# Kernel optimization log

Measured on AMD Instinct MI355X. Metric: run time of the kernel, lower is better.

The kernel has to match this reference:

```python
import jax, jax.numpy as jnp
import numpy as np

N, E = 50000, 800000
IN_DIM, H_DIM, OUT_DIM, EDGE_DIM, HEADS = 128, 128, 112, 8, 1
NEG_SLOPE = 0.2
BN_EPS = 1e-5


def _gat_layer(x, src, dst, edge_att, W, a_src, a_dst, We, a_edge, bias):
    """PyG GATConv (concat=False, edge_dim used for attention only)."""
    H, C = a_src.shape  # heads, out channels
    xs = (x @ W).reshape(-1, H, C)            # [N,H,C]
    ef = (edge_att @ We).reshape(-1, H, C)    # [E,H,C]
    al_src = jnp.einsum('nhc,hc->nh', xs, a_src)   # [N,H]
    al_dst = jnp.einsum('nhc,hc->nh', xs, a_dst)   # [N,H]
    al_edge = jnp.einsum('ehc,hc->eh', ef, a_edge) # [E,H]
    alpha = al_src[src] + al_dst[dst] + al_edge    # [E,H]
    alpha = jnp.where(alpha > 0, alpha, NEG_SLOPE * alpha)  # leaky_relu(0.2)
    # segment softmax over incoming edges of each dst node
    m = jax.lax.stop_gradient(jax.ops.segment_max(alpha, dst, num_segments=N))
    ex = jnp.exp(alpha - m[dst])
    den = jax.ops.segment_sum(ex, dst, num_segments=N)
    att = ex / den[dst]                       # [E,H]
    msg = xs[src] * att[:, :, None]           # [E,H,C] gather + weight
    out = jax.ops.segment_sum(msg, dst, num_segments=N)  # scatter-add [N,H,C]
    return out.mean(axis=1) + bias            # concat=False -> head mean


def _batchnorm(h, gamma, beta):
    mu = h.mean(axis=0)
    var = h.var(axis=0)
    return gamma * (h - mu) * jax.lax.rsqrt(var + BN_EPS) + beta


def setup_inputs() -> dict:
    key = jax.random.key(0)
    ks = jax.random.split(key, 20)
    s = 0.1
    inp = {
        'x': jax.random.normal(ks[0], (N, IN_DIM), dtype=jnp.float32),
        'edge_index': jax.random.randint(ks[1], (2, E), 0, N, dtype=jnp.int32),
        'edge_att': jax.random.normal(ks[2], (E, EDGE_DIM), dtype=jnp.float32),
        # layer 0: IN_DIM -> H_DIM
        'W0': s * jax.random.normal(ks[3], (IN_DIM, HEADS * H_DIM), dtype=jnp.float32),
        'a_src0': s * jax.random.normal(ks[4], (HEADS, H_DIM), dtype=jnp.float32),
        'a_dst0': s * jax.random.normal(ks[5], (HEADS, H_DIM), dtype=jnp.float32),
        'We0': s * jax.random.normal(ks[6], (EDGE_DIM, HEADS * H_DIM), dtype=jnp.float32),
        'a_edge0': s * jax.random.normal(ks[7], (HEADS, H_DIM), dtype=jnp.float32),
        'b0': jnp.zeros((H_DIM,), dtype=jnp.float32),
        # layer 1: H_DIM -> OUT_DIM
        'W1': s * jax.random.normal(ks[8], (H_DIM, HEADS * OUT_DIM), dtype=jnp.float32),
        'a_src1': s * jax.random.normal(ks[9], (HEADS, OUT_DIM), dtype=jnp.float32),
        'a_dst1': s * jax.random.normal(ks[10], (HEADS, OUT_DIM), dtype=jnp.float32),
        'We1': s * jax.random.normal(ks[11], (EDGE_DIM, HEADS * OUT_DIM), dtype=jnp.float32),
        'a_edge1': s * jax.random.normal(ks[12], (HEADS, OUT_DIM), dtype=jnp.float32),
        'b1': jnp.zeros((OUT_DIM,), dtype=jnp.float32),
        # batchnorms
        'bn_g': jnp.ones((H_DIM,), dtype=jnp.float32),
        'bn_b': jnp.zeros((H_DIM,), dtype=jnp.float32),
        'bnf_g': jnp.ones((OUT_DIM,), dtype=jnp.float32),
        'bnf_b': jnp.zeros((OUT_DIM,), dtype=jnp.float32),
    }
    return inp


def reference(x, edge_index, edge_att,
              W0, a_src0, a_dst0, We0, a_edge0, b0,
              W1, a_src1, a_dst1, We1, a_edge1, b1,
              bn_g, bn_b, bnf_g, bnf_b):
    src, dst = edge_index[0], edge_index[1]
    h = _gat_layer(x, src, dst, edge_att, W0, a_src0, a_dst0, We0, a_edge0, b0)
    h = _batchnorm(h, bn_g, bn_b)
    h = jax.nn.relu(h)
    # dropout is a no-op in eval; omitted for a deterministic reference
    h = _gat_layer(h, src, dst, edge_att, W1, a_src1, a_dst1, We1, a_edge1, b1)
    h = _batchnorm(h, bnf_g, bnf_b)
    return h
```

## Files before the change

kernel.cpp:

```cpp
#include <hip/hip_runtime.h>
#include <math.h>

#define NN 50000
#define NPAD 50048
#define NE 800000
#define SCAN_B 256
#define SCAN_NBLK ((NN + SCAN_B - 1) / SCAN_B)
#define AGG_NBLK 3200

typedef __attribute__((ext_vector_type(8))) short bf16x8;
typedef __attribute__((ext_vector_type(4))) float f32x4;
typedef __attribute__((ext_vector_type(8))) unsigned short u16x8;

__device__ __forceinline__ unsigned short f2bf(float x) {
    unsigned u = __float_as_uint(x);
    u += 0x7fffu + ((u >> 16) & 1);
    return (unsigned short)(u >> 16);
}
__device__ __forceinline__ float bf2f(unsigned short h) {
    return __uint_as_float(((unsigned)h) << 16);
}

__global__ void k_init_cvt(int* __restrict__ deg, float* __restrict__ stats,
                           const float* __restrict__ We0, const float* __restrict__ ae0,
                           const float* __restrict__ We1, const float* __restrict__ ae1,
                           float* __restrict__ ve,
                           const float* __restrict__ W0, const float* __restrict__ W1,
                           unsigned short* __restrict__ Wth0, unsigned short* __restrict__ Wtl0,
                           unsigned short* __restrict__ Wth1, unsigned short* __restrict__ Wtl1)
{
    int idx = blockIdx.x * 256 + threadIdx.x;
    if (idx < NN) deg[idx] = 0;
    if (idx < 512) stats[idx] = 0.f;
    if (idx < 128 * 128) {
        int k = idx / 128, c = idx % 128;
        float v = W0[idx];
        unsigned short hi = f2bf(v);
        Wth0[c * 128 + k] = hi;
        Wtl0[c * 128 + k] = f2bf(v - bf2f(hi));
    } else if (idx < 128 * 128 + 128 * 112) {
        int i2 = idx - 128 * 128;
        int k = i2 / 112, c = i2 % 112;
        float v = W1[i2];
        unsigned short hi = f2bf(v);
        Wth1[c * 128 + k] = hi;
        Wtl1[c * 128 + k] = f2bf(v - bf2f(hi));
    }
    if (blockIdx.x == gridDim.x - 1) {
        int j = threadIdx.x;
        if (j < 8) {
            float s = 0.f;
            for (int c = 0; c < 128; ++c) s += We0[j * 128 + c] * ae0[c];
            ve[j] = s;
        } else if (j < 16) {
            int jj = j - 8;
            float s = 0.f;
            for (int c = 0; c < 112; ++c) s += We1[jj * 112 + c] * ae1[c];
            ve[8 + jj] = s;
        }
    }
}

__global__ void k_deg(const int* __restrict__ dst, int* __restrict__ deg,
                      int* __restrict__ rank, int E_)
{
    int e = blockIdx.x * blockDim.x + threadIdx.x;
    if (e < E_) rank[e] = atomicAdd(&deg[dst[e]], 1);
}

__global__ void k_scan1(const int* __restrict__ deg, int* __restrict__ partial)
{
    __shared__ int sm[SCAN_B];
    int t = threadIdx.x;
    int idx = blockIdx.x * SCAN_B + t;
    sm[t] = (idx < NN) ? deg[idx] : 0;
    __syncthreads();
    #pragma unroll
    for (int off = SCAN_B / 2; off > 0; off >>= 1) {
        if (t < off) sm[t] += sm[t + off];
        __syncthreads();
    }
    if (t == 0) partial[blockIdx.x] = sm[0];
}

__global__ void k_scan3(const int* __restrict__ deg, const int* __restrict__ partial,
                        int* __restrict__ rp)
{
    __shared__ int sm[SCAN_B];
    __shared__ int pbase;
    int t = threadIdx.x;
    int pv = (t < SCAN_NBLK && t < blockIdx.x) ? partial[t] : 0;
    sm[t] = pv;
    __syncthreads();
    #pragma unroll
    for (int off = SCAN_B / 2; off > 0; off >>= 1) {
        if (t < off) sm[t] += sm[t + off];
        __syncthreads();
    }
    if (t == 0) pbase = sm[0];
    __syncthreads();
    int idx = blockIdx.x * SCAN_B + t;
    int v = (idx < NN) ? deg[idx] : 0;
    sm[t] = v;
    __syncthreads();
    #pragma unroll
    for (int off = 1; off < SCAN_B; off <<= 1) {
        int u = (t >= off) ? sm[t - off] : 0;
        __syncthreads();
        sm[t] += u;
        __syncthreads();
    }
    int excl = pbase + ((t == 0) ? 0 : sm[t - 1]);
    if (idx < NN) rp[idx] = excl;
    if (idx == NN - 1) rp[NN] = excl + v;
}

__global__ void k_csr_fill_l0(const int* __restrict__ src, const int* __restrict__ dst,
                              const float* __restrict__ eatt, const float* __restrict__ ve,
                              const int* __restrict__ rp, const int* __restrict__ rank,
                              const float* __restrict__ als, const float* __restrict__ ald,
                              uint2* __restrict__ pk, int E_)
{
    int i = blockIdx.x * blockDim.x + threadIdx.x;
    int e = i * 2;
    if (e >= E_) return;
    int2 ss = *reinterpret_cast<const int2*>(src + e);
    int2 dd = *reinterpret_cast<const int2*>(dst + e);
    int2 rr = *reinterpret_cast<const int2*>(rank + e);
    const float4* ea = reinterpret_cast<const float4*>(eatt + (size_t)e * 8);
    float4 ea0 = ea[0], ea1 = ea[1], ea2 = ea[2], ea3 = ea[3];

    float a0x = ea0.x * ve[0] + ea0.y * ve[1] + ea0.z * ve[2] + ea0.w * ve[3]
              + ea1.x * ve[4] + ea1.y * ve[5] + ea1.z * ve[6] + ea1.w * ve[7];
    float a1x = ea0.x * ve[8] + ea0.y * ve[9] + ea0.z * ve[10] + ea0.w * ve[11]
              + ea1.x * ve[12] + ea1.y * ve[13] + ea1.z * ve[14] + ea1.w * ve[15];
    float a0y = ea2.x * ve[0] + ea2.y * ve[1] + ea2.z * ve[2] + ea2.w * ve[3]
              + ea3.x * ve[4] + ea3.y * ve[5] + ea3.z * ve[6] + ea3.w * ve[7];
    float a1y = ea2.x * ve[8] + ea2.y * ve[9] + ea2.z * ve[10] + ea2.w * ve[11]
              + ea3.x * ve[12] + ea3.y * ve[13] + ea3.z * ve[14] + ea3.w * ve[15];

    int p0 = rp[dd.x] + rr.x;
    int p1 = rp[dd.y] + rr.y;
    float lx = als[ss.x] + ald[dd.x] + a0x;
    float ly = als[ss.y] + ald[dd.y] + a0y;
    lx = lx > 0.f ? lx : 0.2f * lx;
    ly = ly > 0.f ? ly : 0.2f * ly;

    uint2 r0, r1;
    r0.x = (unsigned)ss.x | ((unsigned)f2bf(a1x) << 16);
    r0.y = __float_as_uint(__expf(lx));
    r1.x = (unsigned)ss.y | ((unsigned)f2bf(a1y) << 16);
    r1.y = __float_as_uint(__expf(ly));
    pk[p0] = r0;
    pk[p1] = r1;
}

template<int COLS, bool BN_IN>
__launch_bounds__(256, 2)
__global__ void k_gemm_mfma(const float* __restrict__ A,
                            const unsigned short* __restrict__ Wth,
                            const unsigned short* __restrict__ Wtl,
                            unsigned short* __restrict__ out,
                            const float* __restrict__ a_src, const float* __restrict__ a_dst,
                            float* __restrict__ als, float* __restrict__ ald,
                            const float* __restrict__ bsum, const float* __restrict__ bsq,
                            const float* __restrict__ gamma, const float* __restrict__ beta)
{
    constexpr int NT = COLS / 16;
    __shared__ unsigned short sBh[COLS * 128];
    __shared__ unsigned short sBl[COLS * 128];
    __shared__ float scN[128], shN[128];

    int wv = threadIdx.x >> 6;
    int lane = threadIdx.x & 63;
    int r0 = blockIdx.x * 64 + wv * 16;
    int m = lane & 15;
    int quad = lane >> 4;
    int arow = r0 + m;
    int rc = (arow < NN) ? arow : NN - 1;
    const float* pa = A + (size_t)rc * 128 + quad * 8;

    float4 av[8];
    #pragma unroll
    for (int ks = 0; ks < 4; ++ks) {
        av[2 * ks]     = *reinterpret_cast<const float4*>(pa + ks * 32);
        av[2 * ks + 1] = *reinterpret_cast<const float4*>(pa + ks * 32 + 4);
    }

    constexpr int CH = COLS * 128 * 2 / 16;
    for (int i = threadIdx.x; i < CH; i += 256) {
        unsigned o = (unsigned)i * 16u;
        unsigned d = o ^ (((o >> 8) & 7u) << 4);
        *reinterpret_cast<uint4*>(reinterpret_cast<char*>(sBh) + d) =
            *reinterpret_cast<const uint4*>(reinterpret_cast<const char*>(Wth) + o);
        *reinterpret_cast<uint4*>(reinterpret_cast<char*>(sBl) + d) =
            *reinterpret_cast<const uint4*>(reinterpret_cast<const char*>(Wtl) + o);
    }
    if (BN_IN) {
        if (threadIdx.x < 128) {
            int k = threadIdx.x;
            float invn = 1.0f / (float)NN;
            float mean = bsum[k] * invn;
            float var  = bsq[k] * invn - mean * mean;
            float sc = gamma[k] * rsqrtf(var + 1e-5f);
            scN[k] = sc;
            shN[k] = beta[k] - mean * sc;
        }
    }
    __syncthreads();

    f32x4 acc[NT];
    #pragma unroll
    for (int t = 0; t < NT; ++t) acc[t] = f32x4{0.f, 0.f, 0.f, 0.f};

    unsigned swz = ((unsigned)(m & 7)) << 4;

    #pragma unroll
    for (int ks = 0; ks < 4; ++ks) {
        float4 v0 = av[2 * ks], v1 = av[2 * ks + 1];
        float vv[8] = {v0.x, v0.y, v0.z, v0.w, v1.x, v1.y, v1.z, v1.w};
        int kb = ks * 32 + quad * 8;
        bf16x8 ah, al;
        #pragma unroll
        for (int jj = 0; jj < 8; ++jj) {
            float f = vv[jj];
            if (BN_IN) f = fmaxf(f * scN[kb + jj] + shN[kb + jj], 0.f);
            unsigned short hi = f2bf(f);
            ah[jj] = (short)hi;
            al[jj] = (short)f2bf(f - bf2f(hi));
        }
        #pragma unroll
        for (int t = 0; t < NT; ++t) {
            int c = t * 16 + m;
            unsigned b = ((unsigned)c * 256u + (unsigned)ks * 64u + (unsigned)quad * 16u) ^ swz;
            bf16x8 bh = *reinterpret_cast<const bf16x8*>(reinterpret_cast<const char*>(sBh) + b);
            bf16x8 bl = *reinterpret_cast<const bf16x8*>(reinterpret_cast<const char*>(sBl) + b);
            acc[t] = __builtin_amdgcn_mfma_f32_16x16x32_bf16(ah, bh, acc[t], 0, 0, 0);
            acc[t] = __builtin_amdgcn_mfma_f32_16x16x32_bf16(al, bh, acc[t], 0, 0, 0);
            acc[t] = __builtin_amdgcn_mfma_f32_16x16x32_bf16(ah, bl, acc[t], 0, 0, 0);
        }
    }

    float p[4] = {0.f, 0.f, 0.f, 0.f}, q[4] = {0.f, 0.f, 0.f, 0.f};
    #pragma unroll
    for (int t = 0; t < NT; ++t) {
        int c = t * 16 + m;
        float asv = a_src[c], adv = a_dst[c];
        #pragma unroll
        for (int rI = 0; rI < 4; ++rI) {
            float v = acc[t][rI];
            int row = r0 + quad * 4 + rI;
            if (row < NN) out[(size_t)row * COLS + c] = f2bf(v);
            p[rI] += v * asv;
            q[rI] += v * adv;
        }
    }
    #pragma unroll
    for (int rI = 0; rI < 4; ++rI) {
        #pragma unroll
        for (int off = 1; off <= 8; off <<= 1) {
            p[rI] += __shfl_xor(p[rI], off);
            q[rI] += __shfl_xor(q[rI], off);
        }
    }
    if (m == 0) {
        #pragma unroll
        for (int rI = 0; rI < 4; ++rI) {
            int row = r0 + quad * 4 + rI;
            if (row < NN) { als[row] = p[rI]; ald[row] = q[rI]; }
        }
    }
}

__global__ void k_logit1(const int* __restrict__ rp, const uint2* __restrict__ pk,
                         const float* __restrict__ als, const float* __restrict__ ald,
                         uint2* __restrict__ pe1)
{
    int ql = threadIdx.x & 15;
    int w = blockIdx.x * 16 + (threadIdx.x >> 4);
    if (w >= NN) return;
    int beg = rp[w], end = rp[w + 1];
    float aldv = ald[w];
    for (int p = beg + ql; p < end; p += 16) {
        uint2 r = pk[p];
        float a = als[r.x & 0xffffu] + aldv + bf2f((unsigned short)(r.x >> 16));
        a = a > 0.f ? a : 0.2f * a;
        uint2 o;
        o.x = r.x;
        o.y = __float_as_uint(__expf(a));
        pe1[p] = o;
    }
}

template<int COLS>
__global__ void k_aggregate(const int* __restrict__ rp, const uint2* __restrict__ pe,
                            const unsigned short* __restrict__ xs, float* __restrict__ out,
                            float* __restrict__ psum, float* __restrict__ psq)
{
    __shared__ float sS[16 * 128], sQ[16 * 128];
    int ql = threadIdx.x & 15;
    int wq = threadIdx.x >> 4;
    int col = ql * 8;
    bool act = (col < COLS);
    int qid = blockIdx.x * 16 + wq;
    float bs[8] = {0.f,0.f,0.f,0.f,0.f,0.f,0.f,0.f};
    float bq[8] = {0.f,0.f,0.f,0.f,0.f,0.f,0.f,0.f};

    for (int w = qid; w < NN; w += AGG_NBLK * 16) {
        int beg = rp[w], end = rp[w + 1];
        float acc[8] = {0.f,0.f,0.f,0.f,0.f,0.f,0.f,0.f};
        float den = 0.f;
        int j = beg;
        for (; j + 8 <= end; j += 8) {
            uint2 r0 = pe[j],     r1 = pe[j + 1], r2 = pe[j + 2], r3 = pe[j + 3];
            uint2 r4 = pe[j + 4], r5 = pe[j + 5], r6 = pe[j + 6], r7 = pe[j + 7];
            float e0 = __uint_as_float(r0.y), e1 = __uint_as_float(r1.y);
            float e2 = __uint_as_float(r2.y), e3 = __uint_as_float(r3.y);
            float e4 = __uint_as_float(r4.y), e5 = __uint_as_float(r5.y);
            float e6 = __uint_as_float(r6.y), e7 = __uint_as_float(r7.y);
            den += ((e0 + e1) + (e2 + e3)) + ((e4 + e5) + (e6 + e7));
            if (act) {
                u16x8 u0 = *reinterpret_cast<const u16x8*>(xs + (size_t)(r0.x & 0xffffu) * COLS + col);
                u16x8 u1 = *reinterpret_cast<const u16x8*>(xs + (size_t)(r1.x & 0xffffu) * COLS + col);
                u16x8 u2 = *reinterpret_cast<const u16x8*>(xs + (size_t)(r2.x & 0xffffu) * COLS + col);
                u16x8 u3 = *reinterpret_cast<const u16x8*>(xs + (size_t)(r3.x & 0xffffu) * COLS + col);
                u16x8 u4 = *reinterpret_cast<const u16x8*>(xs + (size_t)(r4.x & 0xffffu) * COLS + col);
                u16x8 u5 = *reinterpret_cast<const u16x8*>(xs + (size_t)(r5.x & 0xffffu) * COLS + col);
                u16x8 u6 = *reinterpret_cast<const u16x8*>(xs + (size_t)(r6.x & 0xffffu) * COLS + col);
                u16x8 u7 = *reinterpret_cast<const u16x8*>(xs + (size_t)(r7.x & 0xffffu) * COLS + col);
                #pragma unroll
                for (int k = 0; k < 8; ++k)
                    acc[k] += (((e0 * bf2f(u0[k]) + e1 * bf2f(u1[k]))
                              + (e2 * bf2f(u2[k]) + e3 * bf2f(u3[k])))
                             + ((e4 * bf2f(u4[k]) + e5 * bf2f(u5[k]))
                              + (e6 * bf2f(u6[k]) + e7 * bf2f(u7[k]))));
            }
        }
        if (j < end) {
            bool v1 = j + 1 < end, v2 = j + 2 < end, v3 = j + 3 < end;
            bool v4 = j + 4 < end, v5 = j + 5 < end, v6 = j + 6 < end;
            uint2 r0 = pe[j];
            uint2 r1 = v1 ? pe[j + 1] : uint2{0u, 0u};
            uint2 r2 = v2 ? pe[j + 2] : uint2{0u, 0u};
            uint2 r3 = v3 ? pe[j + 3] : uint2{0u, 0u};
            uint2 r4 = v4 ? pe[j + 4] : uint2{0u, 0u};
            uint2 r5 = v5 ? pe[j + 5] : uint2{0u, 0u};
            uint2 r6 = v6 ? pe[j + 6] : uint2{0u, 0u};
            float e0 = __uint_as_float(r0.y), e1 = __uint_as_float(r1.y);
            float e2 = __uint_as_float(r2.y), e3 = __uint_as_float(r3.y);
            float e4 = __uint_as_float(r4.y), e5 = __uint_as_float(r5.y);
            float e6 = __uint_as_float(r6.y);
            den += ((e0 + e1) + (e2 + e3)) + ((e4 + e5) + e6);
            if (act) {
                u16x8 u0 = *reinterpret_cast<const u16x8*>(xs + (size_t)(r0.x & 0xffffu) * COLS + col);
                #pragma unroll
                for (int k = 0; k < 8; ++k) acc[k] += e0 * bf2f(u0[k]);
                if (v1) {
                    u16x8 u = *reinterpret_cast<const u16x8*>(xs + (size_t)(r1.x & 0xffffu) * COLS + col);
                    #pragma unroll
                    for (int k = 0; k < 8; ++k) acc[k] += e1 * bf2f(u[k]);
                }
                if (v2) {
                    u16x8 u = *reinterpret_cast<const u16x8*>(xs + (size_t)(r2.x & 0xffffu) * COLS + col);
                    #pragma unroll
                    for (int k = 0; k < 8; ++k) acc[k] += e2 * bf2f(u[k]);
                }
                if (v3) {
                    u16x8 u = *reinterpret_cast<const u16x8*>(xs + (size_t)(r3.x & 0xffffu) * COLS + col);
                    #pragma unroll
                    for (int k = 0; k < 8; ++k) acc[k] += e3 * bf2f(u[k]);
                }
                if (v4) {
                    u16x8 u = *reinterpret_cast<const u16x8*>(xs + (size_t)(r4.x & 0xffffu) * COLS + col);
                    #pragma unroll
                    for (int k = 0; k < 8; ++k) acc[k] += e4 * bf2f(u[k]);
                }
                if (v5) {
                    u16x8 u = *reinterpret_cast<const u16x8*>(xs + (size_t)(r5.x & 0xffffu) * COLS + col);
                    #pragma unroll
                    for (int k = 0; k < 8; ++k) acc[k] += e5 * bf2f(u[k]);
                }
                if (v6) {
                    u16x8 u = *reinterpret_cast<const u16x8*>(xs + (size_t)(r6.x & 0xffffu) * COLS + col);
                    #pragma unroll
                    for (int k = 0; k < 8; ++k) acc[k] += e6 * bf2f(u[k]);
                }
            }
        }
        float inv = (end > beg) ? 1.f / den : 0.f;
        if (act) {
            float o[8];
            #pragma unroll
            for (int k = 0; k < 8; ++k) {
                o[k] = acc[k] * inv;
                bs[k] += o[k];
                bq[k] += o[k] * o[k];
            }
            f32x4 o0 = {o[0], o[1], o[2], o[3]};
            f32x4 o1 = {o[4], o[5], o[6], o[7]};
            __builtin_nontemporal_store(o0, reinterpret_cast<f32x4*>(out + (size_t)w * COLS + col));
            __builtin_nontemporal_store(o1, reinterpret_cast<f32x4*>(out + (size_t)w * COLS + col + 4));
        }
    }
    #pragma unroll
    for (int k = 0; k < 8; ++k) {
        sS[wq * 128 + col + k] = act ? bs[k] : 0.f;
        sQ[wq * 128 + col + k] = act ? bq[k] : 0.f;
    }
    __syncthreads();
    int t = threadIdx.x;
    if (t < 128) {
        float s = 0.f, s2 = 0.f;
        #pragma unroll
        for (int r = 0; r < 16; ++r) { s += sS[r * 128 + t]; s2 += sQ[r * 128 + t]; }
        psum[(size_t)blockIdx.x * 128 + t] = s;
        psq [(size_t)blockIdx.x * 128 + t] = s2;
    }
}

__global__ void k_bn_stats2(const float* __restrict__ psum, const float* __restrict__ psq,
                            float* __restrict__ sums, float* __restrict__ sqs)
{
    int t = threadIdx.x;
    int c = t & 127;
    constexpr int ROWS = AGG_NBLK / 128;
    const float* sp = (t < 128) ? psum : psq;
    float s = 0.f;
    #pragma unroll 5
    for (int i = 0; i < ROWS; ++i)
        s += sp[(size_t)(blockIdx.x * ROWS + i) * 128 + c];
    unsafeAtomicAdd(((t < 128) ? sums : sqs) + c, s);
}

template<int COLS>
__global__ void k_bn_apply(const float* __restrict__ in, float* __restrict__ out,
                           const float* __restrict__ sums, const float* __restrict__ sqs,
                           const float* __restrict__ gamma, const float* __restrict__ beta,
                           int n)
{
    int idx = blockIdx.x * blockDim.x + threadIdx.x;
    if (idx >= n * COLS) return;
    int c = idx % COLS;
    float invn = 1.0f / (float)n;
    float mean = sums[c] * invn;
    float var  = sqs[c] * invn - mean * mean;
    float sc = gamma[c] * rsqrtf(var + 1e-5f);
    float sh = beta[c] - mean * sc;
    out[idx] = in[idx] * sc + sh;
}

extern "C" void kernel_launch(void* const* d_in, const int* in_sizes, int n_in,
                              void* d_out, int out_size, void* d_ws, size_t ws_size,
                              hipStream_t stream)
{
    const float* x    = (const float*)d_in[0];
    const int*   eidx = (const int*)d_in[1];
    const float* eatt = (const float*)d_in[2];
    const float* W0   = (const float*)d_in[3];
    const float* as0  = (const float*)d_in[4];
    const float* ad0  = (const float*)d_in[5];
    const float* We0  = (const float*)d_in[6];
    const float* ae0  = (const float*)d_in[7];
    const float* W1   = (const float*)d_in[9];
    const float* as1  = (const float*)d_in[10];
    const float* ad1  = (const float*)d_in[11];
    const float* We1  = (const float*)d_in[12];
    const float* ae1  = (const float*)d_in[13];
    const float* bng  = (const float*)d_in[15];
    const float* bnb  = (const float*)d_in[16];
    const float* bnfg = (const float*)d_in[17];
    const float* bnfb = (const float*)d_in[18];

    const int N = NN, E = NE;
    const int* src = eidx;
    const int* dst = eidx + E;

    float* ws = (float*)d_ws;
    size_t off = 0;
    unsigned short* xs0b = (unsigned short*)(ws + off); off += (size_t)N * 64;
    float* h   = ws + off;      off += (size_t)N * 128;
    unsigned short* xs1b = (unsigned short*)(ws + off); off += (size_t)N * 56;
    uint2* pk = (uint2*)(ws + off);     off += (size_t)E * 2;
    int*   rp   = (int*)(ws + off);     off += N + 2;
    float* als0 = ws + off;     off += N;
    float* ald0 = ws + off;     off += N;
    float* als1 = ws + off;     off += N;
    float* ald1 = ws + off;     off += N;
    float* stats = ws + off;    off += 512;
    float* ve = ws + off;       off += 16;
    int*   partial = (int*)(ws + off);  off += SCAN_NBLK;
    float* psum = ws + off;     off += (size_t)AGG_NBLK * 128;
    float* psq  = ws + off;     off += (size_t)AGG_NBLK * 128;
    unsigned short* Wth0 = (unsigned short*)(ws + off); off += 128 * 64;
    unsigned short* Wtl0 = (unsigned short*)(ws + off); off += 128 * 64;
    unsigned short* Wth1 = (unsigned short*)(ws + off); off += 112 * 64;
    unsigned short* Wtl1 = (unsigned short*)(ws + off); off += 112 * 64;

    int*   rank = (int*)h;
    int*   deg  = (int*)(h + 800000);
    uint2* pe1  = (uint2*)xs0b;
    float* out1 = h;

    float* sum0 = stats;
    float* sq0  = stats + 128;
    float* sum1 = stats + 256;
    float* sq1  = stats + 384;

    k_init_cvt<<<(N + 255) / 256, 256, 0, stream>>>(deg, stats, We0, ae0, We1, ae1, ve,
                                                    W0, W1, Wth0, Wtl0, Wth1, Wtl1);

    k_deg<<<(E + 255) / 256, 256, 0, stream>>>(dst, deg, rank, E);
    k_scan1<<<SCAN_NBLK, SCAN_B, 0, stream>>>(deg, partial);
    k_scan3<<<SCAN_NBLK, SCAN_B, 0, stream>>>(deg, partial, rp);

    k_gemm_mfma<128, false><<<NPAD / 64, 256, 0, stream>>>(x, Wth0, Wtl0, xs0b,
                                                           as0, ad0, als0, ald0,
                                                           nullptr, nullptr, nullptr, nullptr);
    k_csr_fill_l0<<<(E / 2 + 255) / 256, 256, 0, stream>>>(src, dst, eatt, ve, rp, rank,
                                                           als0, ald0, pk, E);
    k_aggregate<128><<<AGG_NBLK, 256, 0, stream>>>(rp, pk, xs0b, h, psum, psq);
    k_bn_stats2<<<128, 256, 0, stream>>>(psum, psq, sum0, sq0);

    k_gemm_mfma<112, true><<<NPAD / 64, 256, 0, stream>>>(h, Wth1, Wtl1, xs1b,
                                                          as1, ad1, als1, ald1,
                                                          sum0, sq0, bng, bnb);
    k_logit1<<<(N + 15) / 16, 256, 0, stream>>>(rp, pk, als1, ald1, pe1);
    k_aggregate<112><<<AGG_NBLK, 256, 0, stream>>>(rp, pe1, xs1b, out1, psum, psq);
    k_bn_stats2<<<128, 256, 0, stream>>>(psum, psq, sum1, sq1);
    k_bn_apply<112><<<(N * 112 + 255) / 256, 256, 0, stream>>>(out1, (float*)d_out, sum1, sq1, bnfg, bnfb, N);
}
```

Before: 345.9 us.

## Fuse edge logits into aggregation and order destination nodes by degree

Edge attention logits and exponentials are now computed inside the aggregation kernels from packed per-edge bf16 edge terms, which removes the separate layer-1 logit kernel and its pe1 buffer. CSR fill no longer depends on the layer-0 GEMM, so it runs before it. The scan kernels also build a degree histogram and a node ordering sorted by descending in-degree, and aggregation processes nodes in that order to balance work across quads. The cost is redundant als gathers and exp work in the aggregate inner loop, plus a scattered ord indirection. The grid now assumes one quad per node with no grid-stride loop.

```diff
diff --git a/kernel.cpp b/kernel.cpp
--- a/kernel.cpp
+++ b/kernel.cpp
@@ -21,7 +21,17 @@
     return __uint_as_float(((unsigned)h) << 16);
 }
 
+template<int LAYER>
+__device__ __forceinline__ float edge_ex(uint2 r, float aldv, const float* __restrict__ als)
+{
+    float ae = bf2f((unsigned short)(LAYER ? (r.y & 0xffffu) : (r.x >> 16)));
+    float a = als[r.x & 0xffffu] + aldv + ae;
+    a = a > 0.f ? a : 0.2f * a;
+    return __expf(a);
+}
+
 __global__ void k_init_cvt(int* __restrict__ deg, float* __restrict__ stats,
+                           int* __restrict__ hist, int* __restrict__ binCur,
                            const float* __restrict__ We0, const float* __restrict__ ae0,
                            const float* __restrict__ We1, const float* __restrict__ ae1,
                            float* __restrict__ ve,
@@ -32,6 +42,7 @@
     int idx = blockIdx.x * 256 + threadIdx.x;
     if (idx < NN) deg[idx] = 0;
     if (idx < 512) stats[idx] = 0.f;
+    if (idx < 64) { hist[idx] = 0; binCur[idx] = 0; }
     if (idx < 128 * 128) {
         int k = idx / 128, c = idx % 128;
         float v = W0[idx];
@@ -68,26 +79,34 @@
     if (e < E_) rank[e] = atomicAdd(&deg[dst[e]], 1);
 }
 
-__global__ void k_scan1(const int* __restrict__ deg, int* __restrict__ partial)
+__global__ void k_scan1(const int* __restrict__ deg, int* __restrict__ partial,
+                        int* __restrict__ hist)
 {
     __shared__ int sm[SCAN_B];
+    __shared__ int lh[64];
     int t = threadIdx.x;
+    if (t < 64) lh[t] = 0;
     int idx = blockIdx.x * SCAN_B + t;
-    sm[t] = (idx < NN) ? deg[idx] : 0;
-    __syncthreads();
+    int d = (idx < NN) ? deg[idx] : 0;
+    sm[t] = d;
+    __syncthreads();
+    if (idx < NN) atomicAdd(&lh[63 - (d < 63 ? d : 63)], 1);
     #pragma unroll
     for (int off = SCAN_B / 2; off > 0; off >>= 1) {
         if (t < off) sm[t] += sm[t + off];
         __syncthreads();
     }
     if (t == 0) partial[blockIdx.x] = sm[0];
+    if (t < 64 && lh[t]) atomicAdd(&hist[t], lh[t]);
 }
 
 __global__ void k_scan3(const int* __restrict__ deg, const int* __restrict__ partial,
-                        int* __restrict__ rp)
+                        int* __restrict__ rp, const int* __restrict__ hist,
+                        int* __restrict__ binCur, int* __restrict__ ord)
 {
     __shared__ int sm[SCAN_B];
     __shared__ int pbase;
+    __shared__ int lh[64], lrsv[64], lstart[64];
     int t = threadIdx.x;
     int pv = (t < SCAN_NBLK && t < blockIdx.x) ? partial[t] : 0;
     sm[t] = pv;
@@ -113,13 +132,29 @@
     int excl = pbase + ((t == 0) ? 0 : sm[t - 1]);
     if (idx < NN) rp[idx] = excl;
     if (idx == NN - 1) rp[NN] = excl + v;
-}
-
-__global__ void k_csr_fill_l0(const int* __restrict__ src, const int* __restrict__ dst,
-                              const float* __restrict__ eatt, const float* __restrict__ ve,
-                              const int* __restrict__ rp, const int* __restrict__ rank,
-                              const float* __restrict__ als, const float* __restrict__ ald,
-                              uint2* __restrict__ pk, int E_)
+
+    if (t < 64) lh[t] = 0;
+    __syncthreads();
+    int b = 0, lr = 0;
+    if (idx < NN) {
+        b = 63 - (v < 63 ? v : 63);
+        lr = atomicAdd(&lh[b], 1);
+    }
+    __syncthreads();
+    if (t < 64) {
+        lrsv[t] = lh[t] ? atomicAdd(&binCur[t], lh[t]) : 0;
+        int s = 0;
+        for (int i = 0; i < t; ++i) s += hist[i];
+        lstart[t] = s;
+    }
+    __syncthreads();
+    if (idx < NN) ord[lstart[b] + lrsv[b] + lr] = idx;
+}
+
+__global__ void k_csr_fill(const int* __restrict__ src, const int* __restrict__ dst,
+                           const float* __restrict__ eatt, const float* __restrict__ ve,
+                           const int* __restrict__ rp, const int* __restrict__ rank,
+                           uint2* __restrict__ pk, int E_)
 {
     int i = blockIdx.x * blockDim.x + threadIdx.x;
     int e = i * 2;
@@ -141,16 +176,11 @@
 
     int p0 = rp[dd.x] + rr.x;
     int p1 = rp[dd.y] + rr.y;
-    float lx = als[ss.x] + ald[dd.x] + a0x;
-    float ly = als[ss.y] + ald[dd.y] + a0y;
-    lx = lx > 0.f ? lx : 0.2f * lx;
-    ly = ly > 0.f ? ly : 0.2f * ly;
-
     uint2 r0, r1;
-    r0.x = (unsigned)ss.x | ((unsigned)f2bf(a1x) << 16);
-    r0.y = __float_as_uint(__expf(lx));
-    r1.x = (unsigned)ss.y | ((unsigned)f2bf(a1y) << 16);
-    r1.y = __float_as_uint(__expf(ly));
+    r0.x = (unsigned)ss.x | ((unsigned)f2bf(a0x) << 16);
+    r0.y = (unsigned)f2bf(a1x);
+    r1.x = (unsigned)ss.y | ((unsigned)f2bf(a0y) << 16);
+    r1.y = (unsigned)f2bf(a1y);
     pk[p0] = r0;
     pk[p1] = r1;
 }
@@ -272,28 +302,10 @@
     }
 }
 
-__global__ void k_logit1(const int* __restrict__ rp, const uint2* __restrict__ pk,
-                         const float* __restrict__ als, const float* __restrict__ ald,
-                         uint2* __restrict__ pe1)
-{
-    int ql = threadIdx.x & 15;
-    int w = blockIdx.x * 16 + (threadIdx.x >> 4);
-    if (w >= NN) return;
-    int beg = rp[w], end = rp[w + 1];
-    float aldv = ald[w];
-    for (int p = beg + ql; p < end; p += 16) {
-        uint2 r = pk[p];
-        float a = als[r.x & 0xffffu] + aldv + bf2f((unsigned short)(r.x >> 16));
-        a = a > 0.f ? a : 0.2f * a;
-        uint2 o;
-        o.x = r.x;
-        o.y = __float_as_uint(__expf(a));
-        pe1[p] = o;
-    }
-}
-
-template<int COLS>
-__global__ void k_aggregate(const int* __restrict__ rp, const uint2* __restrict__ pe,
+template<int COLS, int LAYER>
+__global__ void k_aggregate(const int* __restrict__ rp, const int* __restrict__ ord,
+                            const uint2* __restrict__ pk,
+                            const float* __restrict__ als, const float* __restrict__ ald,
                             const unsigned short* __restrict__ xs, float* __restrict__ out,
                             float* __restrict__ psum, float* __restrict__ psq)
 {
@@ -306,18 +318,20 @@
     float bs[8] = {0.f,0.f,0.f,0.f,0.f,0.f,0.f,0.f};
     float bq[8] = {0.f,0.f,0.f,0.f,0.f,0.f,0.f,0.f};
 
-    for (int w = qid; w < NN; w += AGG_NBLK * 16) {
+    if (qid < NN) {
+        int w = ord[qid];
         int beg = rp[w], end = rp[w + 1];
+        float aldv = ald[w];
         float acc[8] = {0.f,0.f,0.f,0.f,0.f,0.f,0.f,0.f};
         float den = 0.f;
         int j = beg;
         for (; j + 8 <= end; j += 8) {
-            uint2 r0 = pe[j],     r1 = pe[j + 1], r2 = pe[j + 2], r3 = pe[j + 3];
-            uint2 r4 = pe[j + 4], r5 = pe[j + 5], r6 = pe[j + 6], r7 = pe[j + 7];
-            float e0 = __uint_as_float(r0.y), e1 = __uint_as_float(r1.y);
-            float e2 = __uint_as_float(r2.y), e3 = __uint_as_float(r3.y);
-            float e4 = __uint_as_float(r4.y), e5 = __uint_as_float(r5.y);
-            float e6 = __uint_as_float(r6.y), e7 = __uint_as_float(r7.y);
+            uint2 r0 = pk[j],     r1 = pk[j + 1], r2 = pk[j + 2], r3 = pk[j + 3];
+            uint2 r4 = pk[j + 4], r5 = pk[j + 5], r6 = pk[j + 6], r7 = pk[j + 7];
+            float e0 = edge_ex<LAYER>(r0, aldv, als), e1 = edge_ex<LAYER>(r1, aldv, als);
+            float e2 = edge_ex<LAYER>(r2, aldv, als), e3 = edge_ex<LAYER>(r3, aldv, als);
+            float e4 = edge_ex<LAYER>(r4, aldv, als), e5 = edge_ex<LAYER>(r5, aldv, als);
+            float e6 = edge_ex<LAYER>(r6, aldv, als), e7 = edge_ex<LAYER>(r7, aldv, als);
             den += ((e0 + e1) + (e2 + e3)) + ((e4 + e5) + (e6 + e7));
             if (act) {
                 u16x8 u0 = *reinterpret_cast<const u16x8*>(xs + (size_t)(r0.x & 0xffffu) * COLS + col);
@@ -339,17 +353,20 @@
         if (j < end) {
             bool v1 = j + 1 < end, v2 = j + 2 < end, v3 = j + 3 < end;
             bool v4 = j + 4 < end, v5 = j + 5 < end, v6 = j + 6 < end;
-            uint2 r0 = pe[j];
-            uint2 r1 = v1 ? pe[j + 1] : uint2{0u, 0u};
-            uint2 r2 = v2 ? pe[j + 2] : uint2{0u, 0u};
-            uint2 r3 = v3 ? pe[j + 3] : uint2{0u, 0u};
-            uint2 r4 = v4 ? pe[j + 4] : uint2{0u, 0u};
-            uint2 r5 = v5 ? pe[j + 5] : uint2{0u, 0u};
-            uint2 r6 = v6 ? pe[j + 6] : uint2{0u, 0u};
-            float e0 = __uint_as_float(r0.y), e1 = __uint_as_float(r1.y);
-            float e2 = __uint_as_float(r2.y), e3 = __uint_as_float(r3.y);
-            float e4 = __uint_as_float(r4.y), e5 = __uint_as_float(r5.y);
-            float e6 = __uint_as_float(r6.y);
+            uint2 r0 = pk[j];
+            uint2 r1 = v1 ? pk[j + 1] : uint2{0u, 0u};
+            uint2 r2 = v2 ? pk[j + 2] : uint2{0u, 0u};
+            uint2 r3 = v3 ? pk[j + 3] : uint2{0u, 0u};
+            uint2 r4 = v4 ? pk[j + 4] : uint2{0u, 0u};
+            uint2 r5 = v5 ? pk[j + 5] : uint2{0u, 0u};
+            uint2 r6 = v6 ? pk[j + 6] : uint2{0u, 0u};
+            float e0 = edge_ex<LAYER>(r0, aldv, als);
+            float e1 = v1 ? edge_ex<LAYER>(r1, aldv, als) : 0.f;
+            float e2 = v2 ? edge_ex<LAYER>(r2, aldv, als) : 0.f;
+            float e3 = v3 ? edge_ex<LAYER>(r3, aldv, als) : 0.f;
+            float e4 = v4 ? edge_ex<LAYER>(r4, aldv, als) : 0.f;
+            float e5 = v5 ? edge_ex<LAYER>(r5, aldv, als) : 0.f;
+            float e6 = v6 ? edge_ex<LAYER>(r6, aldv, als) : 0.f;
             den += ((e0 + e1) + (e2 + e3)) + ((e4 + e5) + e6);
             if (act) {
                 u16x8 u0 = *reinterpret_cast<const u16x8*>(xs + (size_t)(r0.x & 0xffffu) * COLS + col);
@@ -482,12 +499,15 @@
     unsigned short* xs1b = (unsigned short*)(ws + off); off += (size_t)N * 56;
     uint2* pk = (uint2*)(ws + off);     off += (size_t)E * 2;
     int*   rp   = (int*)(ws + off);     off += N + 2;
+    int*   ord  = (int*)(ws + off);     off += N;
     float* als0 = ws + off;     off += N;
     float* ald0 = ws + off;     off += N;
     float* als1 = ws + off;     off += N;
     float* ald1 = ws + off;     off += N;
     float* stats = ws + off;    off += 512;
     float* ve = ws + off;       off += 16;
+    int*   hist = (int*)(ws + off);     off += 64;
+    int*   binCur = (int*)(ws + off);   off += 64;
     int*   partial = (int*)(ws + off);  off += SCAN_NBLK;
     float* psum = ws + off;     off += (size_t)AGG_NBLK * 128;
     float* psq  = ws + off;     off += (size_t)AGG_NBLK * 128;
@@ -498,7 +518,6 @@
 
     int*   rank = (int*)h;
     int*   deg  = (int*)(h + 800000);
-    uint2* pe1  = (uint2*)xs0b;
     float* out1 = h;
 
     float* sum0 = stats;
@@ -506,26 +525,25 @@
     float* sum1 = stats + 256;
     float* sq1  = stats + 384;
 
-    k_init_cvt<<<(N + 255) / 256, 256, 0, stream>>>(deg, stats, We0, ae0, We1, ae1, ve,
+    k_init_cvt<<<(N + 255) / 256, 256, 0, stream>>>(deg, stats, hist, binCur,
+                                                    We0, ae0, We1, ae1, ve,
                                                     W0, W1, Wth0, Wtl0, Wth1, Wtl1);
 
     k_deg<<<(E + 255) / 256, 256, 0, stream>>>(dst, deg, rank, E);
-    k_scan1<<<SCAN_NBLK, SCAN_B, 0, stream>>>(deg, partial);
-    k_scan3<<<SCAN_NBLK, SCAN_B, 0, stream>>>(deg, partial, rp);
+    k_scan1<<<SCAN_NBLK, SCAN_B, 0, stream>>>(deg, partial, hist);
+    k_scan3<<<SCAN_NBLK, SCAN_B, 0, stream>>>(deg, partial, rp, hist, binCur, ord);
+    k_csr_fill<<<(E / 2 + 255) / 256, 256, 0, stream>>>(src, dst, eatt, ve, rp, rank, pk, E);
 
     k_gemm_mfma<128, false><<<NPAD / 64, 256, 0, stream>>>(x, Wth0, Wtl0, xs0b,
                                                            as0, ad0, als0, ald0,
                                                            nullptr, nullptr, nullptr, nullptr);
-    k_csr_fill_l0<<<(E / 2 + 255) / 256, 256, 0, stream>>>(src, dst, eatt, ve, rp, rank,
-                                                           als0, ald0, pk, E);
-    k_aggregate<128><<<AGG_NBLK, 256, 0, stream>>>(rp, pk, xs0b, h, psum, psq);
+    k_aggregate<128, 0><<<AGG_NBLK, 256, 0, stream>>>(rp, ord, pk, als0, ald0, xs0b, h, psum, psq);
     k_bn_stats2<<<128, 256, 0, stream>>>(psum, psq, sum0, sq0);
 
     k_gemm_mfma<112, true><<<NPAD / 64, 256, 0, stream>>>(h, Wth1, Wtl1, xs1b,
                                                           as1, ad1, als1, ald1,
                                                           sum0, sq0, bng, bnb);
-    k_logit1<<<(N + 15) / 16, 256, 0, stream>>>(rp, pk, als1, ald1, pe1);
-    k_aggregate<112><<<AGG_NBLK, 256, 0, stream>>>(rp, pe1, xs1b, out1, psum, psq);
+    k_aggregate<112, 1><<<AGG_NBLK, 256, 0, stream>>>(rp, ord, pk, als1, ald1, xs1b, out1, psum, psq);
     k_bn_stats2<<<128, 256, 0, stream>>>(psum, psq, sum1, sq1);
     k_bn_apply<112><<<(N * 112 + 255) / 256, 256, 0, stream>>>(out1, (float*)d_out, sum1, sq1, bnfg, bnfb, N);
 }
```

New measurement: 332.4 us. 1.04x faster.
